# Kernel optimization log

Measured on AMD Instinct MI355X. Metric: run time of the kernel, lower is better.

The kernel has to match this reference:

```python
import jax, jax.numpy as jnp
import numpy as np

D_MODEL = 1024
N_HEADS = 16
D_HEAD = D_MODEL // N_HEADS
D_FF = 4096
BATCH = 2
SEQ = 2048
LN_EPS = 1e-5


def setup_inputs() -> dict:
    key = jax.random.key(0)
    ks = jax.random.split(key, 12)
    s = 1.0 / np.sqrt(D_MODEL)
    x = jax.random.normal(ks[0], (BATCH, SEQ, D_MODEL), dtype=jnp.float32)
    mask = jnp.broadcast_to(jnp.tril(jnp.ones((SEQ, SEQ), jnp.int32)), (BATCH, SEQ, SEQ))
    return {
        "x": x,
        "mask": mask,
        # per-head projections stacked: [H, D, Dh] (bias=False in source)
        "Wq": jax.random.normal(ks[1], (N_HEADS, D_MODEL, D_HEAD), jnp.float32) * s,
        "Wk": jax.random.normal(ks[2], (N_HEADS, D_MODEL, D_HEAD), jnp.float32) * s,
        "Wv": jax.random.normal(ks[3], (N_HEADS, D_MODEL, D_HEAD), jnp.float32) * s,
        "Wo": jax.random.normal(ks[4], (D_MODEL, D_MODEL), jnp.float32) * s,
        "ln1_w": jnp.ones((D_MODEL,), jnp.float32),
        "ln1_b": jnp.zeros((D_MODEL,), jnp.float32),
        "ln2_w": jnp.ones((D_MODEL,), jnp.float32),
        "ln2_b": jnp.zeros((D_MODEL,), jnp.float32),
        "W1": jax.random.normal(ks[5], (D_MODEL, D_FF), jnp.float32) * s,
        "b1": jnp.zeros((D_FF,), jnp.float32),
        "W2": jax.random.normal(ks[6], (D_FF, D_MODEL), jnp.float32) * (1.0 / np.sqrt(D_FF)),
        "b2": jnp.zeros((D_MODEL,), jnp.float32),
    }


def layer_norm(x, w, b):
    mu = jnp.mean(x, axis=-1, keepdims=True)
    var = jnp.var(x, axis=-1, keepdims=True)
    return (x - mu) * jax.lax.rsqrt(var + LN_EPS) * w + b


def reference(x, mask, Wq, Wk, Wv, Wo, ln1_w, ln1_b, ln2_w, ln2_b, W1, b1, W2, b2):
    # pre-LN masked self-attention
    h = layer_norm(x, ln1_w, ln1_b)
    q = jnp.einsum("bsd,hde->bhse", h, Wq)  # [B,H,S,Dh]
    k = jnp.einsum("bsd,hde->bhse", h, Wk)
    v = jnp.einsum("bsd,hde->bhse", h, Wv)
    scores = jnp.einsum("bhse,bhte->bhst", q, k) / np.sqrt(D_HEAD)
    scores = jnp.where(mask[:, None, :, :].astype(bool), scores, -jnp.inf)
    weights = jax.nn.softmax(scores, axis=-1)
    attn = jnp.einsum("bhst,bhte->bhse", weights, v)  # [B,H,S,Dh]
    # concat heads (head order = last-dim order in torch.cat)
    concat = attn.transpose(0, 2, 1, 3).reshape(x.shape[0], x.shape[1], D_MODEL)
    att_out = concat @ Wo
    att_x = x + att_out
    # FFN with exact (erf) GELU, matching nn.GELU default
    h2 = layer_norm(att_x, ln2_w, ln2_b)
    ff = jax.nn.gelu(h2 @ W1 + b1, approximate=False) @ W2 + b2
    return att_x + ff
```

## Files before the change

### kernel.cpp

```cpp
#include <hip/hip_runtime.h>
#include <hip/hip_bf16.h>
#include <math.h>

#define D_MODEL 1024
#define N_HEADS 16
#define D_HEAD  64
#define D_FF    4096
#define BATCH   2
#define SEQ     2048
#define NTOK    (BATCH*SEQ)

typedef __hip_bfloat16 bf16;
typedef __attribute__((ext_vector_type(8))) short short8;
typedef __attribute__((ext_vector_type(4))) float floatx4;

template<typename TIN>
__global__ void ln_kernel(const TIN* __restrict__ x,
                          const float* __restrict__ w,
                          const float* __restrict__ b,
                          bf16* __restrict__ out) {
    int row = blockIdx.x;
    int tid = threadIdx.x;
    int wave = tid >> 6, lane = tid & 63;
    const long base = (long)row * D_MODEL;
    float v[4];
    float s = 0.f, sq = 0.f;
#pragma unroll
    for (int i = 0; i < 4; ++i) {
        float xv = (float)x[base + tid + i*256];
        v[i] = xv; s += xv; sq += xv*xv;
    }
#pragma unroll
    for (int m = 32; m >= 1; m >>= 1) {
        s  += __shfl_xor(s,  m, 64);
        sq += __shfl_xor(sq, m, 64);
    }
    __shared__ float r1[4], r2[4];
    if (lane == 0) { r1[wave] = s; r2[wave] = sq; }
    __syncthreads();
    float S  = r1[0] + r1[1] + r1[2] + r1[3];
    float SQ = r2[0] + r2[1] + r2[2] + r2[3];
    float mean = S * (1.f/D_MODEL);
    float var  = SQ * (1.f/D_MODEL) - mean*mean;
    float rstd = rsqrtf(var + 1e-5f);
#pragma unroll
    for (int i = 0; i < 4; ++i) {
        int c = tid + i*256;
        out[base + c] = __float2bfloat16((v[i] - mean) * rstd * w[c] + b[c]);
    }
}

__global__ __launch_bounds__(256) void wcvt_kernel(const float* __restrict__ W,
                                                   bf16* __restrict__ Wt,
                                                   int K, int N) {
    __shared__ float t[32][33];
    int n0 = blockIdx.x * 32, k0 = blockIdx.y * 32;
    int lx = threadIdx.x & 31, ly = threadIdx.x >> 5;
#pragma unroll
    for (int i = 0; i < 4; ++i) {
        int k = ly + i * 8;
        t[k][lx] = W[(long)(k0 + k) * N + n0 + lx];
    }
    __syncthreads();
#pragma unroll
    for (int i = 0; i < 4; ++i) {
        int n = ly + i * 8;
        Wt[(long)(n0 + n) * K + k0 + lx] = __float2bfloat16(t[lx][n]);
    }
}

__global__ __launch_bounds__(256) void wcvt_wo_w1(const float* __restrict__ Wo,
                                                  const float* __restrict__ W1,
                                                  bf16* __restrict__ wo_bf,
                                                  bf16* __restrict__ w1_bf) {
    __shared__ float t[32][33];
    int gx = blockIdx.x;
    const float* W; bf16* Wt; int N, n0;
    if (gx < 32) { W = Wo; Wt = wo_bf; N = D_MODEL; n0 = gx * 32; }
    else         { W = W1; Wt = w1_bf; N = D_FF;    n0 = (gx - 32) * 32; }
    int k0 = blockIdx.y * 32;
    int lx = threadIdx.x & 31, ly = threadIdx.x >> 5;
#pragma unroll
    for (int i = 0; i < 4; ++i) {
        int k = ly + i * 8;
        t[k][lx] = W[(long)(k0 + k) * N + n0 + lx];
    }
    __syncthreads();
#pragma unroll
    for (int i = 0; i < 4; ++i) {
        int n = ly + i * 8;
        Wt[(long)(n0 + n) * D_MODEL + k0 + lx] = __float2bfloat16(t[lx][n]);
    }
}

__global__ __launch_bounds__(256) void wcvt_qkv(const float* __restrict__ Wq,
                                                const float* __restrict__ Wk,
                                                const float* __restrict__ Wv,
                                                bf16* __restrict__ outp) {
    __shared__ float t[32][33];
    int z = blockIdx.z, mat = z >> 4, head = z & 15;
    const float* W = (mat == 0 ? Wq : mat == 1 ? Wk : Wv) + (long)head * D_MODEL * D_HEAD;
    bf16* Wt = outp + (long)z * D_HEAD * D_MODEL;
    int n0 = blockIdx.x * 32, k0 = blockIdx.y * 32;
    int lx = threadIdx.x & 31, ly = threadIdx.x >> 5;
#pragma unroll
    for (int i = 0; i < 4; ++i) {
        int k = ly + i * 8;
        t[k][lx] = W[(long)(k0 + k) * D_HEAD + n0 + lx];
    }
    __syncthreads();
#pragma unroll
    for (int i = 0; i < 4; ++i) {
        int n = ly + i * 8;
        Wt[(long)(n0 + n) * D_MODEL + k0 + lx] = __float2bfloat16(t[lx][n]);
    }
}

__device__ inline void swz2d(int& bx, int& by) {
    int gx = gridDim.x;
    int nwg = gx * gridDim.y;
    int bid = blockIdx.y * gx + blockIdx.x;
    int swz = (bid & 7) * (nwg >> 3) + (bid >> 3);
    bx = swz % gx;
    by = swz / gx;
}

template<int ROWS>
__device__ inline void stage_tile(const bf16* g, int gstride, short* lds) {
    int lane = threadIdx.x & 63, wave = threadIdx.x >> 6;
#pragma unroll
    for (int it = 0; it < ROWS / 64; ++it) {
        int c = wave + it * 4;
        const bf16* gp = g + (long)(c * 16 + (lane >> 2)) * gstride + (lane & 3) * 8;
        short* lp = lds + c * 512 + lane * 8;
        __builtin_amdgcn_global_load_lds(
            (const __attribute__((address_space(1))) void*)gp,
            (__attribute__((address_space(3))) void*)lp, 16, 0, 0);
    }
}

#define G256_BAR  asm volatile("s_barrier" ::: "memory")
#define G256_VM12 asm volatile("s_waitcnt vmcnt(12)" ::: "memory")
#define G256_VM6  asm volatile("s_waitcnt vmcnt(6)" ::: "memory")
#define G256_VM4  asm volatile("s_waitcnt vmcnt(4)" ::: "memory")
#define G256_VM0  asm volatile("s_waitcnt vmcnt(0)" ::: "memory")
#define G256_LGKM0 do { asm volatile("s_waitcnt lgkmcnt(0)" ::: "memory"); \
                        __builtin_amdgcn_sched_barrier(0); } while (0)

__device__ inline short8 rd128(unsigned ad) {
    short8 r;
    asm volatile("ds_read_b128 %0, %1" : "=v"(r) : "v"(ad));
    return r;
}

template<int BM, int BN, int BK, int BIAS, int ACT, int RES, int OUTBF16>
__global__ __launch_bounds__(256) void mfma_gemm_pipe3(
    const bf16* __restrict__ A, int lda,
    const bf16* __restrict__ Wt, int K,
    const float* __restrict__ bias, const float* __restrict__ resid,
    void* __restrict__ Cout, int ldc)
{
    constexpr int MI  = BM / 32;
    constexpr int NR  = BN / 32;
    constexpr int ASZ = BM * BK;
    constexpr int BSZ = BN * BK;
    __shared__ short As[3 * BM * BK];
    __shared__ short Bs[3 * BN * BK];
    int bx, by; swz2d(bx, by);
    int row0 = by * BM, col0 = bx * BN;
    int tid = threadIdx.x, wave = tid >> 6, lane = tid & 63;
    int quad = lane >> 4, l16 = lane & 15;
    int wm = (wave >> 1) * (BM / 2);
    int wn = (wave & 1) * (BN / 2);
    const int NT = K / BK;

    auto stage = [&](int t, int buf) {
        int k0 = t * BK;
#pragma unroll
        for (int kk = 0; kk < BK; kk += 32) {
            stage_tile<BM>(A  + (long)row0 * lda + k0 + kk, lda,
                           As + buf * ASZ + (kk / 32) * BM * 32);
            stage_tile<BN>(Wt + (long)col0 * K   + k0 + kk, K,
                           Bs + buf * BSZ + (kk / 32) * BN * 32);
        }
    };

    unsigned asbase = (unsigned)(unsigned long long)(void*)&As[0];
    unsigned bsbase = (unsigned)(unsigned long long)(void*)&Bs[0];
    unsigned aRow[MI], bRow[NR];
#pragma unroll
    for (int mi = 0; mi < MI; ++mi)
        aRow[mi] = (unsigned)(((wm + mi * 16 + l16) * 32 + quad * 8) * 2);
#pragma unroll
    for (int ni = 0; ni < NR; ++ni)
        bRow[ni] = (unsigned)(((wn + ni * 16 + l16) * 32 + quad * 8) * 2);

    floatx4 acc[MI][NR];
#pragma unroll
    for (int mi = 0; mi < MI; ++mi)
#pragma unroll
        for (int ni = 0; ni < NR; ++ni)
            acc[mi][ni] = (floatx4){0.f, 0.f, 0.f, 0.f};

    stage(0, 0);
    if (NT > 1) stage(1, 1);
    if (NT > 2) stage(2, 2);

    int buf = 0;
    for (int i = 0; i < NT; ++i) {
        if (i + 2 < NT)      { G256_VM12; }
        else if (i + 1 < NT) { G256_VM6;  }
        else                 { G256_VM0;  }
        G256_BAR;

        short8 af[BK / 32][MI], bfr[BK / 32][NR];
#pragma unroll
        for (int p = 0; p < BK / 32; ++p) {
            unsigned ab = asbase + (unsigned)((buf * ASZ + p * BM * 32) * 2);
            unsigned bb = bsbase + (unsigned)((buf * BSZ + p * BN * 32) * 2);
#pragma unroll
            for (int mi = 0; mi < MI; ++mi) af[p][mi] = rd128(ab + aRow[mi]);
#pragma unroll
            for (int ni = 0; ni < NR; ++ni) bfr[p][ni] = rd128(bb + bRow[ni]);
        }
        G256_LGKM0;
#pragma unroll
        for (int p = 0; p < BK / 32; ++p)
#pragma unroll
            for (int mi = 0; mi < MI; ++mi)
#pragma unroll
                for (int ni = 0; ni < NR; ++ni)
                    acc[mi][ni] = __builtin_amdgcn_mfma_f32_16x16x32_bf16(
                        af[p][mi], bfr[p][ni], acc[mi][ni], 0, 0, 0);

        G256_BAR;
        if (i + 3 < NT) stage(i + 3, buf);
        buf = (buf == 2) ? 0 : buf + 1;
    }

#pragma unroll
    for (int mi = 0; mi < MI; ++mi) {
#pragma unroll
        for (int ni = 0; ni < NR; ++ni) {
#pragma unroll
            for (int r = 0; r < 4; ++r) {
                int row = row0 + wm + mi * 16 + quad * 4 + r;
                int col = col0 + wn + ni * 16 + l16;
                float v = acc[mi][ni][r];
                if (BIAS) v += bias[col];
                if (ACT == 1) {
                    float x2 = v * v;
                    float arg = fminf(v * fmaf(0.1029392f, x2, 2.3021182f), 20.f);
                    float t = exp2f(arg);
                    v = v * t * __builtin_amdgcn_rcpf(t + 1.f);
                }
                long idx = (long)row * ldc + col;
                if (RES == 1) v += resid[idx];
                if (OUTBF16) ((bf16*)Cout)[idx] = __float2bfloat16(v);
                else         ((float*)Cout)[idx] = v;
            }
        }
    }
}

struct QkvOut { bf16* o[3]; };

#define RG(buf,mat,kh) (((buf)*4 + (mat)*2 + (kh)) * 8192)

__device__ inline void stage2(const bf16* g0, const bf16* g1, int koff, short* lp) {
    __builtin_amdgcn_global_load_lds(
        (const __attribute__((address_space(1))) void*)(g0 + koff),
        (__attribute__((address_space(3))) void*)lp, 16, 0, 0);
    __builtin_amdgcn_global_load_lds(
        (const __attribute__((address_space(1))) void*)(g1 + koff),
        (__attribute__((address_space(3))) void*)(lp + 4096), 16, 0, 0);
}

template<int MH>
__device__ inline void rd_frags_asm(unsigned ldsbase, int ra, int rb,
                                    const unsigned (&aoff)[8], const unsigned (&boff)[4],
                                    short8 (&areg)[4], short8 (&breg)[4]) {
    if (MH == 0) {
#pragma unroll
        for (int ni = 0; ni < 4; ++ni) {
            unsigned ad = ldsbase + (unsigned)(rb * 2) + boff[ni];
            asm volatile("ds_read_b128 %0, %1" : "=v"(breg[ni]) : "v"(ad));
        }
    }
#pragma unroll
    for (int mi = 0; mi < 4; ++mi) {
        unsigned ad = ldsbase + (unsigned)(ra * 2) + aoff[MH * 4 + mi];
        asm volatile("ds_read_b128 %0, %1" : "=v"(areg[mi]) : "v"(ad));
    }
}

template<int MH>
__device__ inline void do_mfma16(const short8 (&areg)[4], const short8 (&breg)[4],
                                 floatx4 (&acc)[8][4]) {
    __builtin_amdgcn_s_setprio(1);
#pragma unroll
    for (int mi = 0; mi < 4; ++mi)
#pragma unroll
        for (int ni = 0; ni < 4; ++ni)
            acc[MH * 4 + mi][ni] = __builtin_amdgcn_mfma_f32_16x16x32_bf16(
                areg[mi], breg[ni], acc[MH * 4 + mi][ni], 0, 0, 0);
    __builtin_amdgcn_s_setprio(0);
}

template<int EPI>
__global__ __launch_bounds__(512, 1) void gemm256_kernel(
    const bf16* __restrict__ A, int lda,
    const bf16* __restrict__ Wt, int ldw, int K,
    const float* __restrict__ bias,
    bf16* __restrict__ Cout, int ldc, QkvOut qa)
{
    __shared__ short lds[65536];
    const int NT = K / 64;
    int bx, by; swz2d(bx, by);
    int row0 = by * 256, col0 = bx * 256;
    int tid = threadIdx.x;
    int lane = tid & 63, wave = tid >> 6;
    int quad = lane >> 4, l16 = lane & 15;
    int wr = wave >> 2, wc = wave & 3;

    int srow = tid >> 2, slot = tid & 3;
    int cA0 = slot ^ ((srow >> 1) & 3);
    int cA1 = slot ^ (((srow + 128) >> 1) & 3);
    const bf16* a0 = A  + (long)(row0 + srow) * lda + cA0 * 8;
    const bf16* a1 = A  + (long)(row0 + srow + 128) * lda + cA1 * 8;
    const bf16* b0 = Wt + (long)(col0 + srow) * ldw + cA0 * 8;
    const bf16* b1 = Wt + (long)(col0 + srow + 128) * ldw + cA1 * 8;
    short* lt = lds + tid * 8;

    unsigned ldsbase = (unsigned)(unsigned long long)(void*)&lds[0];
    unsigned aoff[8], boff[4];
#pragma unroll
    for (int mi = 0; mi < 8; ++mi) {
        int row = wr * 128 + mi * 16 + l16;
        int sl = quad ^ ((row >> 1) & 3);
        aoff[mi] = (unsigned)((row * 32 + sl * 8) * 2);
    }
#pragma unroll
    for (int ni = 0; ni < 4; ++ni) {
        int row = wc * 64 + ni * 16 + l16;
        int sl = quad ^ ((row >> 1) & 3);
        boff[ni] = (unsigned)((row * 32 + sl * 8) * 2);
    }

    floatx4 acc[8][4];
#pragma unroll
    for (int mi = 0; mi < 8; ++mi)
#pragma unroll
        for (int ni = 0; ni < 4; ++ni)
            acc[mi][ni] = (floatx4){0.f, 0.f, 0.f, 0.f};

    stage2(a0, a1, 0,  lt + RG(0,0,0));
    stage2(b0, b1, 0,  lt + RG(0,1,0));
    stage2(a0, a1, 32, lt + RG(0,0,1));
    stage2(b0, b1, 32, lt + RG(0,1,1));
    stage2(a0, a1, 64, lt + RG(1,0,0));
    stage2(b0, b1, 64, lt + RG(1,1,0));
    G256_VM4;
    G256_BAR;

    short8 areg[4], breg[4];

    for (int i = 0; i < NT / 2; ++i) {
        int T = 2 * i;
        bool s2 = (T + 2 < NT);
        bool s3 = (T + 3 < NT);
        int k1off = (T + 1) * 64;
        int k2off = (T + 2) * 64;
        int k3off = (T + 3) * 64;

        rd_frags_asm<0>(ldsbase, RG(0,0,0), RG(0,1,0), aoff, boff, areg, breg);
        stage2(a0, a1, k1off + 32, lt + RG(1,0,1));
        G256_BAR;
        G256_LGKM0;
        do_mfma16<0>(areg, breg, acc);
        G256_BAR;

        rd_frags_asm<1>(ldsbase, RG(0,0,0), RG(0,1,0), aoff, boff, areg, breg);
        stage2(b0, b1, k1off + 32, lt + RG(1,1,1));
        G256_BAR;
        G256_LGKM0;
        do_mfma16<1>(areg, breg, acc);
        G256_BAR;

        rd_frags_asm<0>(ldsbase, RG(0,0,1), RG(0,1,1), aoff, boff, areg, breg);
        if (s2) stage2(a0, a1, k2off, lt + RG(0,0,0));
        G256_BAR;
        G256_LGKM0;
        do_mfma16<0>(areg, breg, acc);
        G256_BAR;

        rd_frags_asm<1>(ldsbase, RG(0,0,1), RG(0,1,1), aoff, boff, areg, breg);
        if (s2) stage2(b0, b1, k2off, lt + RG(0,1,0));
        G256_BAR;
        G256_LGKM0;
        do_mfma16<1>(areg, breg, acc);
        if (s2) { G256_VM4; } else { G256_VM0; }
        G256_BAR;

        rd_frags_asm<0>(ldsbase, RG(1,0,0), RG(1,1,0), aoff, boff, areg, breg);
        if (s2) stage2(a0, a1, k2off + 32, lt + RG(0,0,1));
        G256_BAR;
        G256_LGKM0;
        do_mfma16<0>(areg, breg, acc);
        G256_BAR;

        rd_frags_asm<1>(ldsbase, RG(1,0,0), RG(1,1,0), aoff, boff, areg, breg);
        if (s2) stage2(b0, b1, k2off + 32, lt + RG(0,1,1));
        G256_BAR;
        G256_LGKM0;
        do_mfma16<1>(areg, breg, acc);
        G256_BAR;

        rd_frags_asm<0>(ldsbase, RG(1,0,1), RG(1,1,1), aoff, boff, areg, breg);
        if (s3) stage2(a0, a1, k3off, lt + RG(1,0,0));
        G256_BAR;
        G256_LGKM0;
        do_mfma16<0>(areg, breg, acc);
        G256_BAR;

        rd_frags_asm<1>(ldsbase, RG(1,0,1), RG(1,1,1), aoff, boff, areg, breg);
        if (s3) stage2(b0, b1, k3off, lt + RG(1,1,0));
        G256_BAR;
        G256_LGKM0;
        do_mfma16<1>(areg, breg, acc);
        if (s3) { G256_VM4; } else { G256_VM0; }
        G256_BAR;
    }

#pragma unroll
    for (int mi = 0; mi < 8; ++mi) {
#pragma unroll
        for (int ni = 0; ni < 4; ++ni) {
#pragma unroll
            for (int r = 0; r < 4; ++r) {
                int row = row0 + wr * 128 + mi * 16 + quad * 4 + r;
                int col = col0 + wc * 64 + ni * 16 + l16;
                float v = acc[mi][ni][r];
                if constexpr (EPI == 0) {
                    v += bias[col];
                    float x2 = v * v;
                    float arg = fminf(v * fmaf(0.1029392f, x2, 2.3021182f), 20.f);
                    float t = exp2f(arg);
                    v = v * t * __builtin_amdgcn_rcpf(t + 1.f);
                    Cout[(long)row * ldc + col] = __float2bfloat16(v);
                } else {
                    int mat = col >> 10, hd = (col >> 6) & 15, d = col & 63;
                    int b = row >> 11, s = row & 2047;
                    qa.o[mat][(((long)(b * 16 + hd) * SEQ + s) << 6) + d] =
                        __float2bfloat16(v);
                }
            }
        }
    }
}

__global__ __launch_bounds__(256) void fattn_mfma(const bf16* __restrict__ q,
                                                  const bf16* __restrict__ k,
                                                  const bf16* __restrict__ v,
                                                  bf16* __restrict__ po,
                                                  float* __restrict__ lz) {
    int byr = blockIdx.y;
    int tile = (byr < 8) ? byr : 23 - byr;
    int chunk = blockIdx.z;
    int bh = blockIdx.x;
    int tid = threadIdx.x;
    int wave = tid >> 6, lane = tid & 63;
    int quad = lane >> 4, l16 = lane & 15;
    const long base = (long)bh * SEQ * D_HEAD;
    const int r0g = tile * 128;

    bf16*  pob = po + (long)chunk * 32 * SEQ * 64;
    float* lzb = lz + (long)chunk * 32 * SEQ;

    __shared__ short Ks[64 * 72];
    __shared__ short Vt[64 * 72];
    __shared__ short Ps[4][32 * 72];

    short8 qf[2][2];
#pragma unroll
    for (int rb = 0; rb < 2; ++rb) {
        const short* qrow = (const short*)(q + base +
            (long)(r0g + wave * 32 + rb * 16 + l16) * D_HEAD);
        qf[rb][0] = *(const short8*)(qrow + quad * 8);
        qf[rb][1] = *(const short8*)(qrow + 32 + quad * 8);
#pragma unroll
        for (int c = 0; c < 2; ++c)
#pragma unroll
            for (int j = 0; j < 8; ++j) {
                float f = __uint_as_float(((unsigned)(unsigned short)qf[rb][c][j]) << 16)
                          * 0.18033688f;
                qf[rb][c][j] = __builtin_bit_cast(short, __float2bfloat16(f));
            }
    }

    short8 onesf;
    {
        short o1 = (l16 == 0) ? (short)0x3F80 : (short)0;
#pragma unroll
        for (int j = 0; j < 8; ++j) onesf[j] = o1;
    }

    floatx4 o[2][4];
#pragma unroll
    for (int rb = 0; rb < 2; ++rb)
#pragma unroll
        for (int nb = 0; nb < 4; ++nb) o[rb][nb] = (floatx4){0.f, 0.f, 0.f, 0.f};
    floatx4 l4[2] = {(floatx4){0.f,0.f,0.f,0.f}, (floatx4){0.f,0.f,0.f,0.f}};

    const int kt0 = chunk ? tile + 1 : 0;
    const int kt1 = chunk ? 2 * tile + 1 : tile;

    uint4 kr0, kr1, va4, vb4;
    auto ldKV = [&](int kt) {
        const short* krow = (const short*)(k + base +
            (long)(kt * 64 + (tid >> 2)) * D_HEAD);
        int c = tid & 3;
        kr0 = *(const uint4*)(krow + c * 16);
        kr1 = *(const uint4*)(krow + c * 16 + 8);
        int tp = (tid & 31) * 2;
        int d0 = ((tid >> 5) & 7) * 8;
        const short* v0 = (const short*)(v + base + (long)(kt * 64 + tp) * D_HEAD + d0);
        va4 = *(const uint4*)v0;
        vb4 = *(const uint4*)(v0 + D_HEAD);
    };

    ldKV(kt0);

    for (int kt = kt0; kt <= kt1; ++kt) {
        __syncthreads();
        {
            int t = tid >> 2, c = tid & 3;
            *(uint4*)&Ks[t * 72 + c * 16]     = kr0;
            *(uint4*)&Ks[t * 72 + c * 16 + 8] = kr1;
        }
        {
            int tp = (tid & 31) * 2;
            int d0 = ((tid >> 5) & 7) * 8;
            short va[8], vb[8];
            *(uint4*)va = va4;
            *(uint4*)vb = vb4;
#pragma unroll
            for (int j = 0; j < 8; ++j) {
                unsigned pk = (unsigned)(unsigned short)va[j] |
                              ((unsigned)(unsigned short)vb[j] << 16);
                *(unsigned*)&Vt[(d0 + j) * 72 + tp] = pk;
            }
        }
        if (kt < kt1) ldKV(kt + 1);
        __syncthreads();

        if (kt * 64 > r0g + wave * 32 + 31) continue;

        floatx4 s[2][4];
        __builtin_amdgcn_s_setprio(1);
#pragma unroll
        for (int nb = 0; nb < 4; ++nb) {
            short8 kf0 = *(const short8*)&Ks[(nb * 16 + l16) * 72 + quad * 8];
            short8 kf1 = *(const short8*)&Ks[(nb * 16 + l16) * 72 + 32 + quad * 8];
#pragma unroll
            for (int rb = 0; rb < 2; ++rb) {
                floatx4 z4 = (floatx4){0.f, 0.f, 0.f, 0.f};
                z4 = __builtin_amdgcn_mfma_f32_16x16x32_bf16(qf[rb][0], kf0, z4, 0, 0, 0);
                z4 = __builtin_amdgcn_mfma_f32_16x16x32_bf16(qf[rb][1], kf1, z4, 0, 0, 0);
                s[rb][nb] = z4;
            }
        }
        __builtin_amdgcn_s_setprio(0);

        if (kt >= 2 * tile) {
#pragma unroll
            for (int rb = 0; rb < 2; ++rb) {
                int qg = r0g + wave * 32 + rb * 16 + quad * 4;
#pragma unroll
                for (int nb = 0; nb < 4; ++nb) {
                    int kg = kt * 64 + nb * 16 + l16;
#pragma unroll
                    for (int r = 0; r < 4; ++r)
                        if (kg > qg + r) s[rb][nb][r] = -1e30f;
                }
            }
        }

        short* Pw = &Ps[wave][0];
#pragma unroll
        for (int rb = 0; rb < 2; ++rb)
#pragma unroll
            for (int nb = 0; nb < 4; ++nb)
#pragma unroll
                for (int r = 0; r < 4; ++r) {
                    float p = exp2f(s[rb][nb][r]);
                    Pw[(rb * 16 + quad * 4 + r) * 72 + nb * 16 + l16] =
                        __builtin_bit_cast(short, __float2bfloat16(p));
                }

        short8 pf[2][2];
#pragma unroll
        for (int rb = 0; rb < 2; ++rb) {
            pf[rb][0] = *(const short8*)&Pw[(rb * 16 + l16) * 72 + quad * 8];
            pf[rb][1] = *(const short8*)&Pw[(rb * 16 + l16) * 72 + 32 + quad * 8];
        }
        __builtin_amdgcn_s_setprio(1);
#pragma unroll
        for (int nb = 0; nb < 4; ++nb) {
            short8 vf0 = *(const short8*)&Vt[(nb * 16 + l16) * 72 + quad * 8];
            short8 vf1 = *(const short8*)&Vt[(nb * 16 + l16) * 72 + 32 + quad * 8];
#pragma unroll
            for (int rb = 0; rb < 2; ++rb) {
                o[rb][nb] = __builtin_amdgcn_mfma_f32_16x16x32_bf16(pf[rb][0], vf0, o[rb][nb], 0, 0, 0);
                o[rb][nb] = __builtin_amdgcn_mfma_f32_16x16x32_bf16(pf[rb][1], vf1, o[rb][nb], 0, 0, 0);
            }
        }
#pragma unroll
        for (int rb = 0; rb < 2; ++rb) {
            l4[rb] = __builtin_amdgcn_mfma_f32_16x16x32_bf16(pf[rb][0], onesf, l4[rb], 0, 0, 0);
            l4[rb] = __builtin_amdgcn_mfma_f32_16x16x32_bf16(pf[rb][1], onesf, l4[rb], 0, 0, 0);
        }
        __builtin_amdgcn_s_setprio(0);
    }

#pragma unroll
    for (int rb = 0; rb < 2; ++rb) {
#pragma unroll
        for (int nb = 0; nb < 4; ++nb)
#pragma unroll
            for (int r = 0; r < 4; ++r) {
                int row = r0g + wave * 32 + rb * 16 + quad * 4 + r;
                pob[((long)bh * SEQ + row) * 64 + nb * 16 + l16] =
                    __float2bfloat16(o[rb][nb][r]);
            }
        if (l16 == 0) {
#pragma unroll
            for (int r = 0; r < 4; ++r) {
                int row = r0g + wave * 32 + rb * 16 + quad * 4 + r;
                lzb[(long)bh * SEQ + row] = l4[rb][r];
            }
        }
    }
}

__global__ __launch_bounds__(256) void attn_combine(const bf16* __restrict__ po,
                                                    const float* __restrict__ lz,
                                                    bf16* __restrict__ cc) {
    const long CH = 32L * SEQ * 64;
    int row = blockIdx.x;
    int b = row >> 11, s = row & 2047;
    int tid = threadIdx.x;
    int col = tid * 4;
    int h = col >> 6, d = col & 63;
    long pidx = ((long)(b * 16 + h) * SEQ + s) * 64 + d;
    uint2 u0 = *(const uint2*)((const unsigned short*)po + pidx);
    uint2 u1 = *(const uint2*)((const unsigned short*)po + CH + pidx);
    long li = (long)(b * 16 + h) * SEQ + s;
    float linv = 1.f / (lz[li] + lz[32L * SEQ + li]);
    unsigned ua[4] = {u0.x & 0xFFFFu, u0.x >> 16, u0.y & 0xFFFFu, u0.y >> 16};
    unsigned ub[4] = {u1.x & 0xFFFFu, u1.x >> 16, u1.y & 0xFFFFu, u1.y >> 16};
    unsigned short rr[4];
#pragma unroll
    for (int i = 0; i < 4; ++i) {
        float ov = __uint_as_float(ua[i] << 16) + __uint_as_float(ub[i] << 16);
        rr[i] = __builtin_bit_cast(unsigned short, __float2bfloat16(ov * linv));
    }
    uint2 w;
    w.x = (unsigned)rr[0] | ((unsigned)rr[1] << 16);
    w.y = (unsigned)rr[2] | ((unsigned)rr[3] << 16);
    *(uint2*)((unsigned short*)cc + (long)row * D_MODEL + col) = w;
}

extern "C" void kernel_launch(void* const* d_in, const int* in_sizes, int n_in,
                              void* d_out, int out_size, void* d_ws, size_t ws_size,
                              hipStream_t stream) {
    const float* x    = (const float*)d_in[0];
    const float* Wq   = (const float*)d_in[2];
    const float* Wk   = (const float*)d_in[3];
    const float* Wv   = (const float*)d_in[4];
    const float* Wo   = (const float*)d_in[5];
    const float* ln1w = (const float*)d_in[6];
    const float* ln1b = (const float*)d_in[7];
    const float* ln2w = (const float*)d_in[8];
    const float* ln2b = (const float*)d_in[9];
    const float* W1   = (const float*)d_in[10];
    const float* b1   = (const float*)d_in[11];
    const float* W2   = (const float*)d_in[12];
    const float* b2   = (const float*)d_in[13];
    float* out = (float*)d_out;

    char* wsb = (char*)d_ws;
    const size_t MB = 1024*1024;
    bf16*  h1      = (bf16*)(wsb + 0*MB);
    bf16*  qb      = (bf16*)(wsb + 8*MB);
    bf16*  kb      = (bf16*)(wsb + 16*MB);
    bf16*  vb      = (bf16*)(wsb + 24*MB);
    bf16*  wqkv_bf = (bf16*)(wsb + 32*MB);
    bf16*  po      = (bf16*)(wsb + 32*MB);
    float* lz      = (float*)(wsb + 48*MB);
    bf16*  cc      = (bf16*)(wsb + 0*MB);
    bf16*  wo_bf   = (bf16*)(wsb + 8*MB);
    bf16*  w1_bf   = (bf16*)(wsb + 10*MB);
    bf16*  h2      = (bf16*)(wsb + 0*MB);
    bf16*  ff      = (bf16*)(wsb + 24*MB);
    bf16*  w2_bf   = (bf16*)(wsb + 8*MB);

    QkvOut qa; qa.o[0] = qb; qa.o[1] = kb; qa.o[2] = vb;
    QkvOut qdummy = {};

    ln_kernel<float><<<NTOK, 256, 0, stream>>>(x, ln1w, ln1b, h1);

    wcvt_qkv<<<dim3(2, 32, 48), 256, 0, stream>>>(Wq, Wk, Wv, wqkv_bf);

    gemm256_kernel<1><<<dim3(12, 16), 512, 0, stream>>>(
        h1, D_MODEL, wqkv_bf, D_MODEL, D_MODEL, nullptr, nullptr, 0, qa);

    fattn_mfma<<<dim3(BATCH*N_HEADS, SEQ/128, 2), 256, 0, stream>>>(qb, kb, vb, po, lz);

    attn_combine<<<NTOK, 256, 0, stream>>>(po, lz, cc);

    wcvt_wo_w1<<<dim3(160, 32), 256, 0, stream>>>(Wo, W1, wo_bf, w1_bf);

    mfma_gemm_pipe3<64,128,64,0,0,1,0><<<dim3(8,64), 256, 0, stream>>>(
        cc, D_MODEL, wo_bf, D_MODEL, nullptr, x, out, D_MODEL);

    ln_kernel<float><<<NTOK, 256, 0, stream>>>(out, ln2w, ln2b, h2);

    gemm256_kernel<0><<<dim3(16, 16), 512, 0, stream>>>(
        h2, D_MODEL, w1_bf, D_MODEL, D_MODEL, b1, ff, D_FF, qdummy);

    wcvt_kernel<<<dim3(D_MODEL/32, D_FF/32), 256, 0, stream>>>(W2, w2_bf, D_FF, D_MODEL);

    mfma_gemm_pipe3<64,128,64,1,0,1,0><<<dim3(8,64), 256, 0, stream>>>(
        ff, D_FF, w2_bf, D_FF, b2, out, out, D_MODEL);
}
```

Baseline: 361.4 us.

## Split causal attention KV range into four chunks for late query tiles

The flash-attention grid changes from a 2-way KV split with paired tiles to a flattened 48-entry y-dimension. Early query tiles (0-7) get 2 KV chunks and late tiles (8-15) get 4 chunks, with work-heavy blocks scheduled first. This is meant to balance per-block work and add parallelism for the long causal rows. The cost is extra partial outputs in a new workspace region, extra reads in the combine kernel for the second half of the sequence, and a reshuffled workspace layout for later buffers.

```diff
diff --git a/kernel.cpp b/kernel.cpp
--- a/kernel.cpp
+++ b/kernel.cpp
@@ -463,22 +463,35 @@
                                                   const bf16* __restrict__ k,
                                                   const bf16* __restrict__ v,
                                                   bf16* __restrict__ po,
+                                                  bf16* __restrict__ po23,
                                                   float* __restrict__ lz) {
-    int byr = blockIdx.y;
-    int tile = (byr < 8) ? byr : 23 - byr;
-    int chunk = blockIdx.z;
+    int yy = 47 - (int)blockIdx.y;
+    int tile, ch, NC;
+    if (yy < 16) { tile = yy >> 1; ch = yy & 1; NC = 2; }
+    else { int z = yy - 16; tile = 8 + (z >> 2); ch = z & 3; NC = 4; }
     int bh = blockIdx.x;
     int tid = threadIdx.x;
     int wave = tid >> 6, lane = tid & 63;
     int quad = lane >> 4, l16 = lane & 15;
     const long base = (long)bh * SEQ * D_HEAD;
     const int r0g = tile * 128;
-
-    bf16*  pob = po + (long)chunk * 32 * SEQ * 64;
-    float* lzb = lz + (long)chunk * 32 * SEQ;
+    const int Vt = 2 * tile + 2;
+    const int kt0 = (ch * Vt) / NC;
+    const int kt1 = ((ch + 1) * Vt) / NC - 1;
+
+    bf16* pob; float* lzb; int rbase;
+    if (ch < 2) {
+        pob = po + (long)ch * 32 * SEQ * 64 + (long)bh * SEQ * 64;
+        lzb = lz + (long)ch * 32 * SEQ + (long)bh * SEQ;
+        rbase = 0;
+    } else {
+        pob = po23 + (long)(ch - 2) * 32 * 1024 * 64 + (long)bh * 1024 * 64;
+        lzb = lz + 64 * SEQ + (long)(ch - 2) * 32 * 1024 + (long)bh * 1024;
+        rbase = 1024;
+    }
 
     __shared__ short Ks[64 * 72];
-    __shared__ short Vt[64 * 72];
+    __shared__ short Vt_[64 * 72];
     __shared__ short Ps[4][32 * 72];
 
     short8 qf[2][2];
@@ -511,9 +524,6 @@
 #pragma unroll
         for (int nb = 0; nb < 4; ++nb) o[rb][nb] = (floatx4){0.f, 0.f, 0.f, 0.f};
     floatx4 l4[2] = {(floatx4){0.f,0.f,0.f,0.f}, (floatx4){0.f,0.f,0.f,0.f}};
-
-    const int kt0 = chunk ? tile + 1 : 0;
-    const int kt1 = chunk ? 2 * tile + 1 : tile;
 
     uint4 kr0, kr1, va4, vb4;
     auto ldKV = [&](int kt) {
@@ -548,7 +558,7 @@
             for (int j = 0; j < 8; ++j) {
                 unsigned pk = (unsigned)(unsigned short)va[j] |
                               ((unsigned)(unsigned short)vb[j] << 16);
-                *(unsigned*)&Vt[(d0 + j) * 72 + tp] = pk;
+                *(unsigned*)&Vt_[(d0 + j) * 72 + tp] = pk;
             }
         }
         if (kt < kt1) ldKV(kt + 1);
@@ -607,8 +617,8 @@
         __builtin_amdgcn_s_setprio(1);
 #pragma unroll
         for (int nb = 0; nb < 4; ++nb) {
-            short8 vf0 = *(const short8*)&Vt[(nb * 16 + l16) * 72 + quad * 8];
-            short8 vf1 = *(const short8*)&Vt[(nb * 16 + l16) * 72 + 32 + quad * 8];
+            short8 vf0 = *(const short8*)&Vt_[(nb * 16 + l16) * 72 + quad * 8];
+            short8 vf1 = *(const short8*)&Vt_[(nb * 16 + l16) * 72 + 32 + quad * 8];
 #pragma unroll
             for (int rb = 0; rb < 2; ++rb) {
                 o[rb][nb] = __builtin_amdgcn_mfma_f32_16x16x32_bf16(pf[rb][0], vf0, o[rb][nb], 0, 0, 0);
@@ -630,23 +640,25 @@
 #pragma unroll
             for (int r = 0; r < 4; ++r) {
                 int row = r0g + wave * 32 + rb * 16 + quad * 4 + r;
-                pob[((long)bh * SEQ + row) * 64 + nb * 16 + l16] =
+                pob[(long)(row - rbase) * 64 + nb * 16 + l16] =
                     __float2bfloat16(o[rb][nb][r]);
             }
         if (l16 == 0) {
 #pragma unroll
             for (int r = 0; r < 4; ++r) {
                 int row = r0g + wave * 32 + rb * 16 + quad * 4 + r;
-                lzb[(long)bh * SEQ + row] = l4[rb][r];
+                lzb[row - rbase] = l4[rb][r];
             }
         }
     }
 }
 
 __global__ __launch_bounds__(256) void attn_combine(const bf16* __restrict__ po,
+                                                    const bf16* __restrict__ po23,
                                                     const float* __restrict__ lz,
                                                     bf16* __restrict__ cc) {
     const long CH = 32L * SEQ * 64;
+    const long CH23 = 32L * 1024 * 64;
     int row = blockIdx.x;
     int b = row >> 11, s = row & 2047;
     int tid = threadIdx.x;
@@ -656,15 +668,30 @@
     uint2 u0 = *(const uint2*)((const unsigned short*)po + pidx);
     uint2 u1 = *(const uint2*)((const unsigned short*)po + CH + pidx);
     long li = (long)(b * 16 + h) * SEQ + s;
-    float linv = 1.f / (lz[li] + lz[32L * SEQ + li]);
+    float lsum = lz[li] + lz[32L * SEQ + li];
     unsigned ua[4] = {u0.x & 0xFFFFu, u0.x >> 16, u0.y & 0xFFFFu, u0.y >> 16};
     unsigned ub[4] = {u1.x & 0xFFFFu, u1.x >> 16, u1.y & 0xFFFFu, u1.y >> 16};
+    float acc[4];
+#pragma unroll
+    for (int i = 0; i < 4; ++i)
+        acc[i] = __uint_as_float(ua[i] << 16) + __uint_as_float(ub[i] << 16);
+    if (s >= 1024) {
+        long p2 = ((long)(b * 16 + h) * 1024 + (s - 1024)) * 64 + d;
+        uint2 u2 = *(const uint2*)((const unsigned short*)po23 + p2);
+        uint2 u3 = *(const uint2*)((const unsigned short*)po23 + CH23 + p2);
+        long l2 = (long)(b * 16 + h) * 1024 + (s - 1024);
+        lsum += lz[64L * SEQ + l2] + lz[64L * SEQ + 32L * 1024 + l2];
+        unsigned uc[4] = {u2.x & 0xFFFFu, u2.x >> 16, u2.y & 0xFFFFu, u2.y >> 16};
+        unsigned ud[4] = {u3.x & 0xFFFFu, u3.x >> 16, u3.y & 0xFFFFu, u3.y >> 16};
+#pragma unroll
+        for (int i = 0; i < 4; ++i)
+            acc[i] += __uint_as_float(uc[i] << 16) + __uint_as_float(ud[i] << 16);
+    }
+    float linv = 1.f / lsum;
     unsigned short rr[4];
 #pragma unroll
-    for (int i = 0; i < 4; ++i) {
-        float ov = __uint_as_float(ua[i] << 16) + __uint_as_float(ub[i] << 16);
-        rr[i] = __builtin_bit_cast(unsigned short, __float2bfloat16(ov * linv));
-    }
+    for (int i = 0; i < 4; ++i)
+        rr[i] = __builtin_bit_cast(unsigned short, __float2bfloat16(acc[i] * linv));
     uint2 w;
     w.x = (unsigned)rr[0] | ((unsigned)rr[1] << 16);
     w.y = (unsigned)rr[2] | ((unsigned)rr[3] << 16);
@@ -697,13 +724,14 @@
     bf16*  vb      = (bf16*)(wsb + 24*MB);
     bf16*  wqkv_bf = (bf16*)(wsb + 32*MB);
     bf16*  po      = (bf16*)(wsb + 32*MB);
+    bf16*  po23    = (bf16*)(wsb + 0*MB);
     float* lz      = (float*)(wsb + 48*MB);
-    bf16*  cc      = (bf16*)(wsb + 0*MB);
-    bf16*  wo_bf   = (bf16*)(wsb + 8*MB);
-    bf16*  w1_bf   = (bf16*)(wsb + 10*MB);
-    bf16*  h2      = (bf16*)(wsb + 0*MB);
+    bf16*  cc      = (bf16*)(wsb + 8*MB);
+    bf16*  wo_bf   = (bf16*)(wsb + 0*MB);
+    bf16*  w1_bf   = (bf16*)(wsb + 16*MB);
+    bf16*  h2      = (bf16*)(wsb + 8*MB);
     bf16*  ff      = (bf16*)(wsb + 24*MB);
-    bf16*  w2_bf   = (bf16*)(wsb + 8*MB);
+    bf16*  w2_bf   = (bf16*)(wsb + 0*MB);
 
     QkvOut qa; qa.o[0] = qb; qa.o[1] = kb; qa.o[2] = vb;
     QkvOut qdummy = {};
@@ -715,9 +743,9 @@
     gemm256_kernel<1><<<dim3(12, 16), 512, 0, stream>>>(
         h1, D_MODEL, wqkv_bf, D_MODEL, D_MODEL, nullptr, nullptr, 0, qa);
 
-    fattn_mfma<<<dim3(BATCH*N_HEADS, SEQ/128, 2), 256, 0, stream>>>(qb, kb, vb, po, lz);
-
-    attn_combine<<<NTOK, 256, 0, stream>>>(po, lz, cc);
+    fattn_mfma<<<dim3(BATCH*N_HEADS, 48), 256, 0, stream>>>(qb, kb, vb, po, po23, lz);
+
+    attn_combine<<<NTOK, 256, 0, stream>>>(po, po23, lz, cc);
 
     wcvt_wo_w1<<<dim3(160, 32), 256, 0, stream>>>(Wo, W1, wo_bf, w1_bf);
 
```

Result: faster. 351.6 us (-2.7%).
